# Kernel optimization log

Measured on AMD Instinct MI355X. Metric: run time of the kernel, lower is better.

## Reference

```python
import jax, jax.numpy as jnp
import numpy as np

N_NODES = 100000
N_REL = 4
N_EDGES = 400000
IN_F, H_F, OUT_F = 128, 128, 64


def setup_inputs() -> dict:
    key = jax.random.key(0)
    ks = jax.random.split(key, 7)
    x = jax.random.normal(ks[0], (N_NODES, IN_F), dtype=jnp.float32)
    src_idx = jax.random.randint(ks[1], (N_REL, N_EDGES), 0, N_NODES, dtype=jnp.int64)
    dst_idx = jax.random.randint(ks[2], (N_REL, N_EDGES), 0, N_NODES, dtype=jnp.int64)
    # Glorot-ish scale for the per-relation GraphConv weights
    W1 = jax.random.normal(ks[3], (N_REL, IN_F, H_F), dtype=jnp.float32) * (1.0 / np.sqrt(IN_F))
    b1 = jnp.zeros((N_REL, H_F), dtype=jnp.float32)
    W2 = jax.random.normal(ks[4], (N_REL, H_F, OUT_F), dtype=jnp.float32) * (1.0 / np.sqrt(H_F))
    b2 = jnp.zeros((N_REL, OUT_F), dtype=jnp.float32)
    return {"x": x, "src_idx": src_idx, "dst_idx": dst_idx,
            "W1": W1, "b1": b1, "W2": W2, "b2": b2}


def _graph_conv(x, src, dst, W, b):
    """DGL GraphConv with norm='both': out = D_in^{-1/2} A^T D_out^{-1/2} x W + b."""
    n = x.shape[0]
    ones = jnp.ones(src.shape[0], dtype=x.dtype)
    deg_out = jnp.maximum(jax.ops.segment_sum(ones, src, num_segments=n), 1.0)
    deg_in = jnp.maximum(jax.ops.segment_sum(ones, dst, num_segments=n), 1.0)
    xn = x * jax.lax.rsqrt(deg_out)[:, None]              # [N, F] src-side norm
    msg = jnp.take(xn, src, axis=0)                        # [E, F] gather
    agg = jax.ops.segment_sum(msg, dst, num_segments=n)   # [N, F] scatter-add
    agg = agg * jax.lax.rsqrt(deg_in)[:, None]            # dst-side norm
    return agg @ W + b


def _hetero_layer(x, src_idx, dst_idx, Ws, bs):
    # per-relation conv, sum-aggregated across relations (HeteroGraphConv 'sum')
    per_rel = jax.vmap(lambda s, d, W, b: _graph_conv(x, s, d, W, b))(src_idx, dst_idx, Ws, bs)
    return per_rel.sum(axis=0)


def reference(x, src_idx, dst_idx, W1, b1, W2, b2):
    h = jax.nn.relu(_hetero_layer(x, src_idx, dst_idx, W1, b1))
    return _hetero_layer(h, src_idx, dst_idx, W2, b2)
```

## Files before the change

kernel.cpp:

```cpp
#include <hip/hip_runtime.h>
#include <hip/hip_bf16.h>

#define NN 100000
#define NR 4
#define NE 400000
#define INF 128
#define HF 128
#define OUTF 64

#define WIN 16384
#define WIN2 (WIN / 2)
#define NWIN 7
#define SUB 16
#define SLICE (NE / SUB)

#define GB 782

#define NBKT 256
#define BKTW 391
#define CAPB 16
#define CAP2 12288
#define EPB 2048
#define SPR 196
#define S1B (NR * SPR)
#define FGRID (GB + S1B)

typedef __attribute__((ext_vector_type(8))) short s16x8;
typedef __attribute__((ext_vector_type(4))) float f32x4;

__global__ __launch_bounds__(256) void deg_win_kernel(const int* __restrict__ src,
                                                      const int* __restrict__ dst,
                                                      unsigned int* __restrict__ parts) {
    __shared__ unsigned int hist[WIN2];
    int arr = blockIdx.z;
    int r   = blockIdx.y;
    int win = blockIdx.x / SUB;
    int sub = blockIdx.x % SUB;
    const int4* idx4 = (const int4*)((arr ? dst : src) + (size_t)r * NE + (size_t)sub * SLICE);
    int base = win * WIN;

    uint4 z4 = make_uint4(0, 0, 0, 0);
    for (int i = threadIdx.x; i < WIN2 / 4; i += 256) ((uint4*)hist)[i] = z4;
    __syncthreads();

    auto proc = [&](int4 v) {
        int a;
        a = v.x - base; if ((unsigned)a < WIN) atomicAdd(&hist[a >> 1], 1u << ((a & 1) << 4));
        a = v.y - base; if ((unsigned)a < WIN) atomicAdd(&hist[a >> 1], 1u << ((a & 1) << 4));
        a = v.z - base; if ((unsigned)a < WIN) atomicAdd(&hist[a >> 1], 1u << ((a & 1) << 4));
        a = v.w - base; if ((unsigned)a < WIN) atomicAdd(&hist[a >> 1], 1u << ((a & 1) << 4));
    };

    constexpr int NV = SLICE / 4;
    int i = threadIdx.x;
    for (; i + 256 < NV; i += 512) {
        int4 va = idx4[i];
        int4 vb = idx4[i + 256];
        proc(va);
        proc(vb);
    }
    if (i < NV) proc(idx4[i]);
    __syncthreads();

    unsigned int* outp = parts + ((((size_t)arr * NR + r) * NWIN + win) * SUB + sub) * WIN2;
    for (int j = threadIdx.x; j < WIN2 / 4; j += 256)
        ((uint4*)outp)[j] = ((const uint4*)hist)[j];
}

__global__ void red_norm_kernel(const unsigned int* __restrict__ parts, int* __restrict__ deg_tot,
                                float* __restrict__ rno, float* __restrict__ rni) {
    int n = blockIdx.x * blockDim.x + threadIdx.x;
    if (n >= NN) return;
    if (n == 0) deg_tot[NN] = 0;
    int win = n / WIN, off = n % WIN;
    int word = off >> 1, sh = (off & 1) << 4;
    int tot = 0;
    #pragma unroll
    for (int r = 0; r < NR; r++) {
        const unsigned int* p0 = parts + (((size_t)0 * NR + r) * NWIN + win) * SUB * WIN2 + word;
        const unsigned int* p1 = parts + (((size_t)1 * NR + r) * NWIN + win) * SUB * WIN2 + word;
        int so = 0, si = 0;
        #pragma unroll
        for (int s = 0; s < SUB; s++) {
            so += (p0[(size_t)s * WIN2] >> sh) & 0xFFFFu;
            si += (p1[(size_t)s * WIN2] >> sh) & 0xFFFFu;
        }
        rno[(size_t)r * NN + n] = rsqrtf(fmaxf((float)so, 1.0f));
        rni[(size_t)r * NN + n] = rsqrtf(fmaxf((float)si, 1.0f));
        tot += si;
    }
    deg_tot[n] = tot;
}

__global__ void scan_block_kernel(const int* __restrict__ in, int* __restrict__ out,
                                  int* __restrict__ blockSums, int n) {
    __shared__ int sd[256];
    int t = threadIdx.x;
    int base = blockIdx.x * 1024 + t * 4;
    int v[4];
    #pragma unroll
    for (int j = 0; j < 4; j++) v[j] = (base + j < n) ? ((in[base + j] + 7) & ~7) : 0;
    int ts = v[0] + v[1] + v[2] + v[3];
    sd[t] = ts;
    __syncthreads();
    int acc = ts;
    for (int off = 1; off < 256; off <<= 1) {
        int x = (t >= off) ? sd[t - off] : 0;
        __syncthreads();
        acc += x; sd[t] = acc;
        __syncthreads();
    }
    int run = acc - ts;
    #pragma unroll
    for (int j = 0; j < 4; j++) {
        if (base + j < n) out[base + j] = run;
        run += v[j];
    }
    if (t == 255) blockSums[blockIdx.x] = acc;
}

__global__ void scan_sums_kernel(int* __restrict__ blockSums, int nb) {
    __shared__ int sd[512];
    int t = threadIdx.x;
    int v = (t < nb) ? blockSums[t] : 0;
    sd[t] = v;
    __syncthreads();
    int acc = v;
    for (int off = 1; off < 512; off <<= 1) {
        int x = (t >= off) ? sd[t - off] : 0;
        __syncthreads();
        acc += x; sd[t] = acc;
        __syncthreads();
    }
    if (t < nb) blockSums[t] = acc - v;
}

__global__ void scan_add_kernel(int* __restrict__ row_ptr, const int* __restrict__ blockSums,
                                int* __restrict__ bcur, int n) {
    int i = blockIdx.x * blockDim.x + threadIdx.x;
    if (i < n) {
        int v = row_ptr[i] + blockSums[i >> 10];
        row_ptr[i] = v;
        if (i < NN && (i % BKTW) == 0) bcur[i / BKTW] = v;
    }
}

__global__ void prep_kernel(const float* __restrict__ W1, const float* __restrict__ W2,
                            const float* __restrict__ b1, const float* __restrict__ b2,
                            __hip_bfloat16* __restrict__ Wt1, __hip_bfloat16* __restrict__ Wt2,
                            float* __restrict__ bsum1, float* __restrict__ bsum2) {
    if (blockIdx.x == 384) {
        int t = threadIdx.x;
        if (t < HF) {
            float s = 0.f;
            for (int r = 0; r < NR; r++) s += b1[r * HF + t];
            bsum1[t] = s;
        } else if (t < HF + OUTF) {
            int f = t - HF;
            float s = 0.f;
            for (int r = 0; r < NR; r++) s += b2[r * OUTF + f];
            bsum2[f] = s;
        }
        return;
    }
    int id = blockIdx.x * 256 + threadIdx.x;
    if (id < NR * HF * INF) {
        int r = id >> 14, rem = id & 16383;
        int n_ = rem >> 7, k = rem & 127;
        Wt1[id] = __float2bfloat16(W1[((size_t)r * INF + k) * HF + n_]);
    } else {
        int id2 = id - NR * HF * INF;
        if (id2 < NR * OUTF * HF) {
            int r = id2 >> 13, rem = id2 & 8191;
            int n_ = rem >> 7, k = rem & 127;
            Wt2[id2] = __float2bfloat16(W2[((size_t)r * HF + k) * OUTF + n_]);
        }
    }
}

__device__ __forceinline__ s16x8 pack_bf16x8(float4 a0, float4 a1) {
    union { s16x8 v; __hip_bfloat162 h[4]; } u;
    u.h[0] = __float22bfloat162_rn(make_float2(a0.x, a0.y));
    u.h[1] = __float22bfloat162_rn(make_float2(a0.z, a0.w));
    u.h[2] = __float22bfloat162_rn(make_float2(a1.x, a1.y));
    u.h[3] = __float22bfloat162_rn(make_float2(a1.z, a1.w));
    return u.v;
}

__device__ __forceinline__ void load_lds_16(const void* g, void* l) {
    __builtin_amdgcn_global_load_lds(
        (const __attribute__((address_space(1))) void*)g,
        (__attribute__((address_space(3))) void*)l, 16, 0, 0);
}

template<int F, typename AT>
__device__ __forceinline__ void gemm_body(int mbase, const AT* __restrict__ Xb,
                                          const __hip_bfloat16* __restrict__ Wt,
                                          __hip_bfloat16* __restrict__ Zb, int nrel,
                                          __hip_bfloat16* Bs) {
    constexpr int NT = F / 16;
    constexpr int NG = F * 16;

    int tid  = threadIdx.x;
    int wid  = tid >> 6;
    int lane = tid & 63;
    int quad = lane >> 4;
    int l16  = lane & 15;
    int sw   = l16 & 7;

    int bofs[4];
    #pragma unroll
    for (int kb = 0; kb < 4; kb++)
        bofs[kb] = l16 * 256 + (((kb * 4 + quad) ^ sw) << 4);

    s16x8 afr[2][4];
    #pragma unroll
    for (int mt = 0; mt < 2; mt++) {
        int mrow = mbase + mt * 64 + wid * 16 + l16;
        if (mrow >= NN) mrow = NN - 1;
        #pragma unroll
        for (int kb = 0; kb < 4; kb++) {
            if constexpr (sizeof(AT) == 4) {
                const float* xr = (const float*)Xb + (size_t)mrow * 128 + kb * 32 + quad * 8;
                float4 a0 = *(const float4*)xr;
                float4 a1 = *(const float4*)(xr + 4);
                afr[mt][kb] = pack_bf16x8(a0, a1);
            } else {
                afr[mt][kb] = *(const s16x8*)((const __hip_bfloat16*)Xb + (size_t)mrow * 128 + kb * 32 + quad * 8);
            }
        }
    }

    for (int rel = 0; rel < nrel; rel++) {
        if (rel) __syncthreads();

        {
            const char* W = (const char*)(Wt + (size_t)rel * F * 128);
            #pragma unroll
            for (int it = 0; it < NG / 256; it++) {
                int dg = it * 256 + tid;
                int sg = dg ^ ((dg >> 4) & 7);
                load_lds_16(W + (size_t)sg * 16, (char*)Bs + (size_t)(dg & ~63) * 16);
            }
        }
        __syncthreads();

        __hip_bfloat16* Z = Zb + (size_t)rel * NN * F;

        f32x4 acc[2][NT];
        #pragma unroll
        for (int nt = 0; nt < NT; nt++) {
            acc[0][nt] = (f32x4){0.f, 0.f, 0.f, 0.f};
            acc[1][nt] = (f32x4){0.f, 0.f, 0.f, 0.f};
            #pragma unroll
            for (int kb = 0; kb < 4; kb++) {
                s16x8 bfr = *(const s16x8*)((const char*)Bs + nt * 4096 + bofs[kb]);
                acc[0][nt] = __builtin_amdgcn_mfma_f32_16x16x32_bf16(bfr, afr[0][kb], acc[0][nt], 0, 0, 0);
                acc[1][nt] = __builtin_amdgcn_mfma_f32_16x16x32_bf16(bfr, afr[1][kb], acc[1][nt], 0, 0, 0);
            }
        }

        #pragma unroll
        for (int mt = 0; mt < 2; mt++) {
            int g = mbase + mt * 64 + wid * 16 + l16;
            if (g < NN) {
                #pragma unroll
                for (int nt = 0; nt < NT; nt++) {
                    union { uint2 u; __hip_bfloat162 h[2]; } o;
                    o.h[0] = __float22bfloat162_rn(make_float2(acc[mt][nt][0], acc[mt][nt][1]));
                    o.h[1] = __float22bfloat162_rn(make_float2(acc[mt][nt][2], acc[mt][nt][3]));
                    *(uint2*)(Z + (size_t)g * F + nt * 16 + quad * 4) = o.u;
                }
            }
        }
    }
}

__global__ __launch_bounds__(256, 3) void fusedC_kernel(
        const float* __restrict__ x, const __hip_bfloat16* __restrict__ Wt1,
        __hip_bfloat16* __restrict__ Zb,
        const int* __restrict__ src, const int* __restrict__ dst,
        int* __restrict__ bcur, unsigned int* __restrict__ temp) {
    __shared__ __attribute__((aligned(16))) char sm[HF * 128 * 2];
    int b = blockIdx.x;
    if ((b & 1) == 0 && (b >> 1) < GB) {
        gemm_body<HF, float>((b >> 1) * 128, x, Wt1, Zb, NR, (__hip_bfloat16*)sm);
        return;
    }
    int sb = (b & 1) ? (b >> 1) : (S1B - 1);
    unsigned int (*lbuf)[CAPB] = (unsigned int(*)[CAPB])sm;
    int* cur = (int*)(sm + NBKT * CAPB * 4);

    int r = sb / SPR;
    int q = sb % SPR;
    int base_e = q * EPB;
    int n = NE - base_e; if (n > EPB) n = EPB;
    int tid = threadIdx.x;
    cur[tid] = 0;
    __syncthreads();

    if (tid * 8 < n) {
        const int4* sp4 = (const int4*)(src + (size_t)r * NE + base_e);
        const int4* dp4 = (const int4*)(dst + (size_t)r * NE + base_e);
        int4 s0 = sp4[tid * 2], s1 = sp4[tid * 2 + 1];
        int4 d0 = dp4[tid * 2], d1 = dp4[tid * 2 + 1];
        auto one = [&](int s, int d) {
            unsigned k = (unsigned)d / BKTW;
            int dlo = d - (int)k * BKTW;
            unsigned rec = ((unsigned)(r * NN + s) << 9) | (unsigned)dlo;
            int pos = atomicAdd(&cur[k], 1);
            if (pos < CAPB) lbuf[k][pos] = rec;
            else temp[atomicAdd(&bcur[k], 1)] = rec;
        };
        one(s0.x, d0.x); one(s0.y, d0.y); one(s0.z, d0.z); one(s0.w, d0.w);
        one(s1.x, d1.x); one(s1.y, d1.y); one(s1.z, d1.z); one(s1.w, d1.w);
    }
    __syncthreads();

    int c = cur[tid]; if (c > CAPB) c = CAPB;
    if (c) {
        int g = atomicAdd(&bcur[tid], c);
        for (int j = 0; j < c; j++) temp[g + j] = lbuf[tid][j];
    }
}

__global__ __launch_bounds__(256) void pass2_kernel(const int* __restrict__ bcur,
                                                    const unsigned int* __restrict__ temp,
                                                    const int* __restrict__ row_ptr,
                                                    const float* __restrict__ rno,
                                                    const float* __restrict__ rni,
                                                    int2* __restrict__ edges) {
    __shared__ __attribute__((aligned(16))) int2 stg[CAP2];
    __shared__ int cur[BKTW + 1];
    int k   = blockIdx.x;
    int D0  = k * BKTW;
    int ND  = NN - D0; if (ND > BKTW) ND = BKTW;
    int base = row_ptr[D0];
    int span = row_ptr[D0 + ND] - base;
    int cnt  = bcur[k] - base;
    int tid  = threadIdx.x;

    if (span <= CAP2) {
        int4 z = make_int4(0, 0, 0, 0);
        for (int j = tid; j < (span >> 1); j += 256) ((int4*)stg)[j] = z;
        for (int i = tid; i < ND; i += 256) cur[i] = row_ptr[D0 + i] - base;
        __syncthreads();
        for (int j = tid; j < cnt; j += 256) {
            unsigned rec = temp[base + j];
            int dlo = rec & 511;
            unsigned idx = rec >> 9;
            int p = atomicAdd(&cur[dlo], 1);
            float c = rno[idx] * rni[(size_t)(idx / NN) * NN + D0 + dlo];
            stg[p] = make_int2((int)(idx << 8), __float_as_int(c));
        }
        __syncthreads();
        int4* dq = (int4*)(edges + base);
        const int4* sq = (const int4*)stg;
        for (int j = tid; j < (span >> 1); j += 256) dq[j] = sq[j];
    } else {
        int4 z = make_int4(0, 0, 0, 0);
        int4* dq = (int4*)(edges + base);
        for (int j = tid; j < (span >> 1); j += 256) dq[j] = z;
        for (int i = tid; i < ND; i += 256) cur[i] = row_ptr[D0 + i];
        __syncthreads();
        for (int j = tid; j < cnt; j += 256) {
            unsigned rec = temp[base + j];
            int dlo = rec & 511;
            unsigned idx = rec >> 9;
            int p = atomicAdd(&cur[dlo], 1);
            float c = rno[idx] * rni[(size_t)(idx / NN) * NN + D0 + dlo];
            edges[p] = make_int2((int)(idx << 8), __float_as_int(c));
        }
    }
}

template<int F, typename AT>
__global__ __launch_bounds__(256, 3) void gemm_all(const AT* __restrict__ Xb,
                                                   const __hip_bfloat16* __restrict__ Wt,
                                                   __hip_bfloat16* __restrict__ Zb, int nrel) {
    __shared__ __attribute__((aligned(16))) __hip_bfloat16 Bs[F * 128];
    gemm_body<F, AT>(blockIdx.x * 128, Xb, Wt, Zb, nrel, Bs);
}

template<int F, bool RELU, bool OUT_F32>
__global__ __launch_bounds__(256) void gather_merged(const int* __restrict__ row_ptr,
                              const int2* __restrict__ edges,
                              const __hip_bfloat16* __restrict__ Zb,
                              float* __restrict__ outf, __hip_bfloat16* __restrict__ outb,
                              const float* __restrict__ bsum) {
    int wid  = threadIdx.x >> 6;
    int lane = threadIdx.x & 63;
    int n = blockIdx.x * 4 + wid;
    int beg = row_ptr[n];
    int end = row_ptr[n + 1];

    if constexpr (F == 128) {
        const char* Zl = (const char*)Zb + lane * 4;
        float2 a = *(const float2*)(bsum + lane * 2);
        for (int p = beg; p < end; p += 8) {
            int2 e[8];
            #pragma unroll
            for (int j = 0; j < 8; j++) e[j] = edges[p + j];
            float2 zz[8];
            #pragma unroll
            for (int j = 0; j < 8; j++)
                zz[j] = __bfloat1622float2(*(const __hip_bfloat162*)(Zl + e[j].x));
            #pragma unroll
            for (int j = 0; j < 8; j++) {
                float c = __int_as_float(e[j].y);
                a.x = fmaf(c, zz[j].x, a.x);
                a.y = fmaf(c, zz[j].y, a.y);
            }
        }
        if constexpr (RELU) { a.x = fmaxf(a.x, 0.f); a.y = fmaxf(a.y, 0.f); }
        *(__hip_bfloat162*)(outb + (size_t)n * 128 + lane * 2) = __float22bfloat162_rn(a);
    } else {
        const char* Zl = (const char*)Zb + lane * 2;
        float a = bsum[lane];
        for (int p = beg; p < end; p += 8) {
            int2 e[8];
            #pragma unroll
            for (int j = 0; j < 8; j++) e[j] = edges[p + j];
            float zz[8];
            #pragma unroll
            for (int j = 0; j < 8; j++)
                zz[j] = __bfloat162float(*(const __hip_bfloat16*)(Zl + (e[j].x >> 1)));
            #pragma unroll
            for (int j = 0; j < 8; j++) a = fmaf(__int_as_float(e[j].y), zz[j], a);
        }
        if constexpr (RELU) a = fmaxf(a, 0.f);
        if constexpr (OUT_F32) outf[(size_t)n * 64 + lane] = a;
        else outb[(size_t)n * 64 + lane] = __float2bfloat16(a);
    }
}

extern "C" void kernel_launch(void* const* d_in, const int* in_sizes, int n_in,
                              void* d_out, int out_size, void* d_ws, size_t ws_size,
                              hipStream_t stream) {
    const float* x   = (const float*)d_in[0];
    const int*   src = (const int*)  d_in[1];
    const int*   dst = (const int*)  d_in[2];
    const float* W1  = (const float*)d_in[3];
    const float* b1  = (const float*)d_in[4];
    const float* W2  = (const float*)d_in[5];
    const float* b2  = (const float*)d_in[6];
    float* out = (float*)d_out;

    constexpr int RN = NR * NN;
    constexpr int NSC = NN + 1;
    constexpr int NB = (NSC + 1023) / 1024;

    char* p = (char*)d_ws;
    int*   deg_tot   = (int*)p;   p += ((size_t)NN + 16) * 4;
    float* rno       = (float*)p; p += (size_t)RN * 4;
    float* rni       = (float*)p; p += (size_t)RN * 4;
    int*   row_ptr   = (int*)p;   p += ((size_t)NN + 16) * 4;
    int*   cursor    = (int*)p;   p += (size_t)NN * 4;
    int*   blockSums = (int*)p;   p += 1024 * 4;
    int2*  edges     = (int2*)p;  p += ((size_t)NR * NE + 8 * NN) * 8;
    float* bsum1 = (float*)p; p += HF * 4;
    float* bsum2 = (float*)p; p += OUTF * 4;
    __hip_bfloat16* hb  = (__hip_bfloat16*)p; p += (size_t)NN * HF * 2;
    __hip_bfloat16* Wt1 = (__hip_bfloat16*)p; p += (size_t)NR * HF * INF * 2;
    __hip_bfloat16* Wt2 = (__hip_bfloat16*)p; p += (size_t)NR * OUTF * HF * 2;
    __hip_bfloat16* Zb = (__hip_bfloat16*)p;
    unsigned int* parts = (unsigned int*)Zb;
    int* bcur = blockSums + 512;
    unsigned int* temp = (unsigned int*)hb;

    prep_kernel<<<385, 256, 0, stream>>>(W1, W2, b1, b2, Wt1, Wt2, bsum1, bsum2);
    deg_win_kernel<<<dim3(NWIN * SUB, NR, 2), 256, 0, stream>>>(src, dst, parts);
    red_norm_kernel<<<(NN + 255) / 256, 256, 0, stream>>>(parts, deg_tot, rno, rni);
    scan_block_kernel<<<NB, 256, 0, stream>>>(deg_tot, row_ptr, blockSums, NSC);
    scan_sums_kernel<<<1, 512, 0, stream>>>(blockSums, NB);
    scan_add_kernel<<<(NSC + 255) / 256, 256, 0, stream>>>(row_ptr, blockSums, bcur, NSC);

    fusedC_kernel<<<FGRID, 256, 0, stream>>>(x, Wt1, Zb, src, dst, bcur, temp);

    pass2_kernel<<<NBKT, 256, 0, stream>>>(bcur, temp, row_ptr, rno, rni, edges);

    constexpr int GG = NN / 4;

    gather_merged<HF, true, false><<<GG, 256, 0, stream>>>(
        row_ptr, edges, Zb, nullptr, hb, bsum1);

    gemm_all<OUTF, __hip_bfloat16><<<GB, 256, 0, stream>>>(hb, Wt2, Zb, 4);
    gather_merged<OUTF, false, true><<<GG, 256, 0, stream>>>(
        row_ptr, edges, Zb, out, nullptr, bsum2);
}
```

Measured before the change: 370.5 us.

## Replace global bucket cursors with fixed per-block bucket cells and overflow list

The edge bucketing pass now writes each block's records straight into a fixed-size per-(block,bucket) cell in global memory, with a byte count per cell. This drops the staging through shared memory and the global atomic cursor per bucket. Records past cell capacity go to a single global overflow list. Pass2 then walks all cells for its bucket and scans the whole overflow list, filtering by bucket. In exchange pass2 does more strided, uncoalesced reads, and every block scans the full overflow list.

```diff
diff --git a/kernel.cpp b/kernel.cpp
--- a/kernel.cpp
+++ b/kernel.cpp
@@ -136,13 +136,10 @@
 }
 
 __global__ void scan_add_kernel(int* __restrict__ row_ptr, const int* __restrict__ blockSums,
-                                int* __restrict__ bcur, int n) {
+                                int* __restrict__ ovfcnt, int n) {
     int i = blockIdx.x * blockDim.x + threadIdx.x;
-    if (i < n) {
-        int v = row_ptr[i] + blockSums[i >> 10];
-        row_ptr[i] = v;
-        if (i < NN && (i % BKTW) == 0) bcur[i / BKTW] = v;
-    }
+    if (i < n) row_ptr[i] = row_ptr[i] + blockSums[i >> 10];
+    if (i == 0) ovfcnt[0] = 0;
 }
 
 __global__ void prep_kernel(const float* __restrict__ W1, const float* __restrict__ W2,
@@ -280,17 +277,20 @@
         const float* __restrict__ x, const __hip_bfloat16* __restrict__ Wt1,
         __hip_bfloat16* __restrict__ Zb,
         const int* __restrict__ src, const int* __restrict__ dst,
-        int* __restrict__ bcur, unsigned int* __restrict__ temp) {
+        unsigned int* __restrict__ temp, unsigned char* __restrict__ cnt,
+        int* __restrict__ ovfcnt, int2* __restrict__ ovf) {
     __shared__ __attribute__((aligned(16))) char sm[HF * 128 * 2];
     int b = blockIdx.x;
-    if ((b & 1) == 0 && (b >> 1) < GB) {
-        gemm_body<HF, float>((b >> 1) * 128, x, Wt1, Zb, NR, (__hip_bfloat16*)sm);
-        return;
-    }
-    int sb = (b & 1) ? (b >> 1) : (S1B - 1);
-    unsigned int (*lbuf)[CAPB] = (unsigned int(*)[CAPB])sm;
-    int* cur = (int*)(sm + NBKT * CAPB * 4);
-
+    int sb;
+    if (b < 2 * GB) {
+        if ((b & 1) == 0) {
+            gemm_body<HF, float>((b >> 1) * 128, x, Wt1, Zb, NR, (__hip_bfloat16*)sm);
+            return;
+        }
+        sb = b >> 1;
+    } else sb = b - GB;
+
+    int* cur = (int*)sm;
     int r = sb / SPR;
     int q = sb % SPR;
     int base_e = q * EPB;
@@ -309,8 +309,10 @@
             int dlo = d - (int)k * BKTW;
             unsigned rec = ((unsigned)(r * NN + s) << 9) | (unsigned)dlo;
             int pos = atomicAdd(&cur[k], 1);
-            if (pos < CAPB) lbuf[k][pos] = rec;
-            else temp[atomicAdd(&bcur[k], 1)] = rec;
+            if (pos < CAPB)
+                temp[((size_t)sb * NBKT + k) * CAPB + pos] = rec;
+            else
+                ovf[atomicAdd(ovfcnt, 1)] = make_int2((int)k, (int)rec);
         };
         one(s0.x, d0.x); one(s0.y, d0.y); one(s0.z, d0.z); one(s0.w, d0.w);
         one(s1.x, d1.x); one(s1.y, d1.y); one(s1.z, d1.z); one(s1.w, d1.w);
@@ -318,14 +320,13 @@
     __syncthreads();
 
     int c = cur[tid]; if (c > CAPB) c = CAPB;
-    if (c) {
-        int g = atomicAdd(&bcur[tid], c);
-        for (int j = 0; j < c; j++) temp[g + j] = lbuf[tid][j];
-    }
-}
-
-__global__ __launch_bounds__(256) void pass2_kernel(const int* __restrict__ bcur,
-                                                    const unsigned int* __restrict__ temp,
+    cnt[(size_t)sb * NBKT + tid] = (unsigned char)c;
+}
+
+__global__ __launch_bounds__(256) void pass2_kernel(const unsigned int* __restrict__ temp,
+                                                    const unsigned char* __restrict__ cnt,
+                                                    const int* __restrict__ ovfcnt,
+                                                    const int2* __restrict__ ovf,
                                                     const int* __restrict__ row_ptr,
                                                     const float* __restrict__ rno,
                                                     const float* __restrict__ rni,
@@ -337,21 +338,36 @@
     int ND  = NN - D0; if (ND > BKTW) ND = BKTW;
     int base = row_ptr[D0];
     int span = row_ptr[D0 + ND] - base;
-    int cnt  = bcur[k] - base;
     int tid  = threadIdx.x;
+    int novf = ovfcnt[0];
 
     if (span <= CAP2) {
         int4 z = make_int4(0, 0, 0, 0);
         for (int j = tid; j < (span >> 1); j += 256) ((int4*)stg)[j] = z;
         for (int i = tid; i < ND; i += 256) cur[i] = row_ptr[D0 + i] - base;
         __syncthreads();
-        for (int j = tid; j < cnt; j += 256) {
-            unsigned rec = temp[base + j];
-            int dlo = rec & 511;
-            unsigned idx = rec >> 9;
-            int p = atomicAdd(&cur[dlo], 1);
-            float c = rno[idx] * rni[(size_t)(idx / NN) * NN + D0 + dlo];
-            stg[p] = make_int2((int)(idx << 8), __float_as_int(c));
+        for (int j = tid; j < S1B; j += 256) {
+            int c = cnt[(size_t)j * NBKT + k];
+            const unsigned int* cell = temp + ((size_t)j * NBKT + k) * CAPB;
+            for (int i = 0; i < c; i++) {
+                unsigned rec = cell[i];
+                int dlo = rec & 511;
+                unsigned idx = rec >> 9;
+                int p = atomicAdd(&cur[dlo], 1);
+                float cf = rno[idx] * rni[(size_t)(idx / NN) * NN + D0 + dlo];
+                stg[p] = make_int2((int)(idx << 8), __float_as_int(cf));
+            }
+        }
+        for (int o = tid; o < novf; o += 256) {
+            int2 e = ovf[o];
+            if (e.x == k) {
+                unsigned rec = (unsigned)e.y;
+                int dlo = rec & 511;
+                unsigned idx = rec >> 9;
+                int p = atomicAdd(&cur[dlo], 1);
+                float cf = rno[idx] * rni[(size_t)(idx / NN) * NN + D0 + dlo];
+                stg[p] = make_int2((int)(idx << 8), __float_as_int(cf));
+            }
         }
         __syncthreads();
         int4* dq = (int4*)(edges + base);
@@ -363,13 +379,28 @@
         for (int j = tid; j < (span >> 1); j += 256) dq[j] = z;
         for (int i = tid; i < ND; i += 256) cur[i] = row_ptr[D0 + i];
         __syncthreads();
-        for (int j = tid; j < cnt; j += 256) {
-            unsigned rec = temp[base + j];
-            int dlo = rec & 511;
-            unsigned idx = rec >> 9;
-            int p = atomicAdd(&cur[dlo], 1);
-            float c = rno[idx] * rni[(size_t)(idx / NN) * NN + D0 + dlo];
-            edges[p] = make_int2((int)(idx << 8), __float_as_int(c));
+        for (int j = tid; j < S1B; j += 256) {
+            int c = cnt[(size_t)j * NBKT + k];
+            const unsigned int* cell = temp + ((size_t)j * NBKT + k) * CAPB;
+            for (int i = 0; i < c; i++) {
+                unsigned rec = cell[i];
+                int dlo = rec & 511;
+                unsigned idx = rec >> 9;
+                int p = atomicAdd(&cur[dlo], 1);
+                float cf = rno[idx] * rni[(size_t)(idx / NN) * NN + D0 + dlo];
+                edges[p] = make_int2((int)(idx << 8), __float_as_int(cf));
+            }
+        }
+        for (int o = tid; o < novf; o += 256) {
+            int2 e = ovf[o];
+            if (e.x == k) {
+                unsigned rec = (unsigned)e.y;
+                int dlo = rec & 511;
+                unsigned idx = rec >> 9;
+                int p = atomicAdd(&cur[dlo], 1);
+                float cf = rno[idx] * rni[(size_t)(idx / NN) * NN + D0 + dlo];
+                edges[p] = make_int2((int)(idx << 8), __float_as_int(cf));
+            }
         }
     }
 }
@@ -463,21 +494,23 @@
     __hip_bfloat16* hb  = (__hip_bfloat16*)p; p += (size_t)NN * HF * 2;
     __hip_bfloat16* Wt1 = (__hip_bfloat16*)p; p += (size_t)NR * HF * INF * 2;
     __hip_bfloat16* Wt2 = (__hip_bfloat16*)p; p += (size_t)NR * OUTF * HF * 2;
-    __hip_bfloat16* Zb = (__hip_bfloat16*)p;
+    __hip_bfloat16* Zb = (__hip_bfloat16*)p; p += (size_t)NR * NN * HF * 2;
+    int2* ovf = (int2*)p; p += (size_t)NR * NE * 8;
     unsigned int* parts = (unsigned int*)Zb;
-    int* bcur = blockSums + 512;
     unsigned int* temp = (unsigned int*)hb;
+    unsigned char* cnt = (unsigned char*)hb + (size_t)S1B * NBKT * CAPB * 4;
+    int* ovfcnt = blockSums + 512;
 
     prep_kernel<<<385, 256, 0, stream>>>(W1, W2, b1, b2, Wt1, Wt2, bsum1, bsum2);
     deg_win_kernel<<<dim3(NWIN * SUB, NR, 2), 256, 0, stream>>>(src, dst, parts);
     red_norm_kernel<<<(NN + 255) / 256, 256, 0, stream>>>(parts, deg_tot, rno, rni);
     scan_block_kernel<<<NB, 256, 0, stream>>>(deg_tot, row_ptr, blockSums, NSC);
     scan_sums_kernel<<<1, 512, 0, stream>>>(blockSums, NB);
-    scan_add_kernel<<<(NSC + 255) / 256, 256, 0, stream>>>(row_ptr, blockSums, bcur, NSC);
-
-    fusedC_kernel<<<FGRID, 256, 0, stream>>>(x, Wt1, Zb, src, dst, bcur, temp);
-
-    pass2_kernel<<<NBKT, 256, 0, stream>>>(bcur, temp, row_ptr, rno, rni, edges);
+    scan_add_kernel<<<(NSC + 255) / 256, 256, 0, stream>>>(row_ptr, blockSums, ovfcnt, NSC);
+
+    fusedC_kernel<<<FGRID, 256, 0, stream>>>(x, Wt1, Zb, src, dst, temp, cnt, ovfcnt, ovf);
+
+    pass2_kernel<<<NBKT, 256, 0, stream>>>(temp, cnt, ovfcnt, ovf, row_ptr, rno, rni, edges);
 
     constexpr int GG = NN / 4;
 
```

Result: no change. 376.6 us (+1.6%).
